# Kernel tuning notes

Measured on AMD Instinct MI355X. Metric: run time of the kernel, lower is better.

Reference implementation:

```python
import jax, jax.numpy as jnp
import numpy as np

N, E = 100000, 1200000
IN, HC = 3, 64
FC1, FC2, FC3, OUT = 64, 32, 16, 3
BN_EPS = 1e-5


def _lin(key, fan_in, fan_out):
    # kaiming-uniform-ish init, zero bias (as in parameter_init)
    bound = np.sqrt(6.0 / fan_in)
    w = jax.random.uniform(key, (fan_in, fan_out), minval=-bound, maxval=bound, dtype=jnp.float32)
    return w, jnp.zeros((fan_out,), jnp.float32)


def setup_inputs() -> dict:
    key = jax.random.key(0)
    ks = jax.random.split(key, 16)
    x = jax.random.normal(ks[0], (N, IN), dtype=jnp.float32)
    edge_index = jax.random.randint(ks[1], (2, E), 0, N, dtype=jnp.int64)
    d = {"x": x, "edge_index": edge_index}
    # EdgeConv MLPs: Linear(2*c_in, hc) -> ReLU -> Linear(hc, hc)
    d["w1a"], d["b1a"] = _lin(ks[2], 2 * IN, HC)
    d["w1b"], d["b1b"] = _lin(ks[3], HC, HC)
    d["w2a"], d["b2a"] = _lin(ks[4], 2 * HC, HC)
    d["w2b"], d["b2b"] = _lin(ks[5], HC, HC)
    d["w3a"], d["b3a"] = _lin(ks[6], 2 * HC, HC)
    d["w3b"], d["b3b"] = _lin(ks[7], HC, HC)
    # BatchNorm (eval mode) params per layer: gamma, beta, running_mean, running_var
    for i in (1, 2, 3):
        d[f"bn{i}_g"] = jnp.ones((HC,), jnp.float32)
        d[f"bn{i}_b"] = jnp.zeros((HC,), jnp.float32)
        d[f"bn{i}_m"] = jnp.zeros((HC,), jnp.float32)
        d[f"bn{i}_v"] = jnp.ones((HC,), jnp.float32)
    # dense head
    d["lw1"], d["lb1"] = _lin(ks[8], HC, FC1)
    d["lw2"], d["lb2"] = _lin(ks[9], FC1, FC2)
    d["lw3"], d["lb3"] = _lin(ks[10], FC2, FC3)
    d["lw4"], d["lb4"] = _lin(ks[11], FC3, OUT)
    return d


def _edge_conv(x, src, dst, wa, ba, wb, bb):
    # PyG EdgeConv: message = mlp(cat[x_i, x_j - x_i]), max-aggregated at target i
    x_i = x[dst]                              # [E, C]
    x_j = x[src]                              # [E, C]
    h = jnp.concatenate([x_i, x_j - x_i], axis=-1)   # [E, 2C]
    h = jax.nn.relu(h @ wa + ba) @ wb + bb           # [E, HC]
    agg = jax.ops.segment_max(h, dst, num_segments=x.shape[0])
    return jnp.where(jnp.isfinite(agg), agg, 0.0)    # isolated nodes -> 0


def _bn(x, g, b, m, v):
    return (x - m) * jax.lax.rsqrt(v + BN_EPS) * g + b


def reference(x, edge_index,
              w1a, b1a, w1b, b1b, w2a, b2a, w2b, b2b, w3a, b3a, w3b, b3b,
              bn1_g, bn1_b, bn1_m, bn1_v, bn2_g, bn2_b, bn2_m, bn2_v,
              bn3_g, bn3_b, bn3_m, bn3_v,
              lw1, lb1, lw2, lb2, lw3, lb3, lw4, lb4):
    src, dst = edge_index[0], edge_index[1]
    h = _edge_conv(x, src, dst, w1a, b1a, w1b, b1b)
    h = jax.nn.relu(_bn(h, bn1_g, bn1_b, bn1_m, bn1_v))
    h = _edge_conv(h, src, dst, w2a, b2a, w2b, b2b)
    h = jax.nn.relu(_bn(h, bn2_g, bn2_b, bn2_m, bn2_v))
    h = _edge_conv(h, src, dst, w3a, b3a, w3b, b3b)
    h = jax.nn.relu(_bn(h, bn3_g, bn3_b, bn3_m, bn3_v))
    h = jax.nn.relu(h @ lw1 + lb1)
    h = jax.nn.relu(h @ lw2 + lb2)
    h = jax.nn.relu(h @ lw3 + lb3)
    return h @ lw4 + lb4
```

## Files before the change

kernel.cpp:

```cpp
#include <hip/hip_runtime.h>

#define CAP 64
#define BN_EPS 1e-5f

typedef _Float16 f16;
typedef _Float16 half8 __attribute__((ext_vector_type(8)));
typedef float f32x4 __attribute__((ext_vector_type(4)));

__global__ __launch_bounds__(256) void build_buckets(
    const int* __restrict__ ei, int E,
    int* __restrict__ deg, int* __restrict__ bucket)
{
    int e = blockIdx.x * blockDim.x + threadIdx.x;
    if (e >= E) return;
    int src = ei[e];
    int dst = ei[E + e];
    int slot = atomicAdd(&deg[dst], 1);
    if (slot < CAP) bucket[dst * CAP + slot] = src;
}

__global__ __launch_bounds__(256) void uv_kernel(
    const float* __restrict__ feat, int ldf, int K, int N,
    const float* __restrict__ wa, const float* __restrict__ ba,
    f16* __restrict__ U, f16* __restrict__ V)
{
    __shared__ float Wlds[2][64][64];
    __shared__ float blds[64];
    int tid = threadIdx.x;
    for (int idx = tid; idx < 2 * K * 64; idx += blockDim.x) {
        int half = idx / (K * 64);
        int rem = idx - half * (K * 64);
        int k = rem >> 6, o = rem & 63;
        float wB = wa[(K + k) * 64 + o];
        Wlds[half][k][o] = (half == 0) ? (wa[k * 64 + o] - wB) : wB;
    }
    if (tid < 64) blds[tid] = ba[tid];
    __syncthreads();

    int t = blockIdx.x * blockDim.x + tid;
    if (t >= 2 * N) return;
    int node = t >> 1, half = t & 1;

    float acc[64];
    #pragma unroll
    for (int o = 0; o < 64; ++o) acc[o] = (half == 0) ? blds[o] : 0.f;

    const float* f = feat + (long)node * ldf;
    for (int k = 0; k < K; ++k) {
        float c = f[k];
        #pragma unroll
        for (int o = 0; o < 64; ++o) acc[o] = fmaf(c, Wlds[half][k][o], acc[o]);
    }
    f16* dstp = (half == 0 ? U : V) + (long)node * 64;
    #pragma unroll
    for (int o = 0; o < 64; o += 8) {
        half8 h;
        #pragma unroll
        for (int j = 0; j < 8; ++j) h[j] = (f16)acc[o + j];
        *(half8*)(dstp + o) = h;
    }
}

__global__ __launch_bounds__(256) void node_kernel(
    const f16* __restrict__ U, const f16* __restrict__ V,
    const int* __restrict__ deg, const int* __restrict__ bucket,
    const float* __restrict__ wb, const float* __restrict__ bb,
    const float* __restrict__ bng, const float* __restrict__ bnb,
    const float* __restrict__ bnm, const float* __restrict__ bnv,
    int N, float* __restrict__ Fout)
{
    const int lane = threadIdx.x & 63;
    const int r16 = lane >> 4, c16 = lane & 15;
    const int wid = (blockIdx.x * blockDim.x + threadIdx.x) >> 6;
    const int nwaves = (gridDim.x * blockDim.x) >> 6;

    half8 bfrag[8];
    #pragma unroll
    for (int ct = 0; ct < 4; ++ct)
        #pragma unroll
        for (int s = 0; s < 2; ++s) {
            half8 h;
            #pragma unroll
            for (int j = 0; j < 8; ++j) {
                int k = 32 * s + 8 * r16 + j;
                h[j] = (f16)wb[k * 64 + 16 * ct + c16];
            }
            bfrag[ct * 2 + s] = h;
        }

    const float bbv = bb[lane];
    const float g = bng[lane], be = bnb[lane];
    const float rs = rsqrtf(bnv[lane] + BN_EPS), mm = bnm[lane];

    int chunk = (N + nwaves - 1) / nwaves;
    int n0 = wid * chunk;
    int n1 = n0 + chunk; if (n1 > N) n1 = N;
    if (n0 >= n1) return;

    int dval = 0;
    if (lane < n1 - n0) dval = deg[n0 + lane];
    dval = dval > CAP ? CAP : dval;

    int bkt_cur = bucket[(long)n0 * CAP + c16];
    int np = (n0 + 1 < n1) ? n0 + 1 : n0;
    int bkt_nxt = bucket[(long)np * CAP + c16];

    unsigned s0u = (unsigned)bkt_cur < (unsigned)N ? (unsigned)bkt_cur : 0u;
    const half8* vr = (const half8*)(V + (long)s0u * 64);
    half8 vA = vr[r16], vB = vr[4 + r16];
    const half8* ur = (const half8*)(U + (long)n0 * 64);
    half8 uA = ur[r16], uB = ur[4 + r16];

    for (int node = n0; node < n1; ++node) {
        unsigned s1u = (unsigned)bkt_nxt < (unsigned)N ? (unsigned)bkt_nxt : 0u;
        const half8* vr1 = (const half8*)(V + (long)s1u * 64);
        half8 vA2 = vr1[r16], vB2 = vr1[4 + r16];
        int nn = (node + 2 < n1) ? node + 2 : n1 - 1;
        int bkt_fut = bucket[(long)nn * CAP + c16];
        int np1 = (node + 1 < n1) ? node + 1 : node;
        const half8* ur1 = (const half8*)(U + (long)np1 * 64);
        half8 uA2 = ur1[r16], uB2 = ur1[4 + r16];

        int d = __shfl(dval, node - n0);

        float m0 = -INFINITY, m1 = -INFINITY, m2 = -INFINITY, m3 = -INFINITY;
        int ntile = (d + 15) >> 4;

        if (ntile > 0) {
            half8 a0 = vA + uA;
            half8 a1 = vB + uB;
            #pragma unroll
            for (int j = 0; j < 8; ++j) {
                a0[j] = a0[j] > (f16)0 ? a0[j] : (f16)0;
                a1[j] = a1[j] > (f16)0 ? a1[j] : (f16)0;
            }
            const f32x4 z = {0.f, 0.f, 0.f, 0.f};
            #pragma unroll
            for (int ct = 0; ct < 4; ++ct) {
                f32x4 acc = __builtin_amdgcn_mfma_f32_16x16x32_f16(a0, bfrag[ct * 2 + 0], z, 0, 0, 0);
                acc = __builtin_amdgcn_mfma_f32_16x16x32_f16(a1, bfrag[ct * 2 + 1], acc, 0, 0, 0);
                float mx = -INFINITY;
                #pragma unroll
                for (int r = 0; r < 4; ++r) {
                    int row = r16 * 4 + r;
                    float val = (row < d) ? acc[r] : -INFINITY;
                    mx = fmaxf(mx, val);
                }
                mx = fmaxf(mx, __shfl_xor(mx, 16));
                mx = fmaxf(mx, __shfl_xor(mx, 32));
                if (ct == 0) m0 = fmaxf(m0, mx);
                else if (ct == 1) m1 = fmaxf(m1, mx);
                else if (ct == 2) m2 = fmaxf(m2, mx);
                else m3 = fmaxf(m3, mx);
            }
        }
        for (int t = 1; t < ntile; ++t) {
            int bkt = bucket[(long)node * CAP + t * 16 + c16];
            unsigned su = (unsigned)bkt < (unsigned)N ? (unsigned)bkt : 0u;
            const half8* vrt = (const half8*)(V + (long)su * 64);
            half8 a0 = vrt[r16] + uA;
            half8 a1 = vrt[4 + r16] + uB;
            #pragma unroll
            for (int j = 0; j < 8; ++j) {
                a0[j] = a0[j] > (f16)0 ? a0[j] : (f16)0;
                a1[j] = a1[j] > (f16)0 ? a1[j] : (f16)0;
            }
            const f32x4 z = {0.f, 0.f, 0.f, 0.f};
            #pragma unroll
            for (int ct = 0; ct < 4; ++ct) {
                f32x4 acc = __builtin_amdgcn_mfma_f32_16x16x32_f16(a0, bfrag[ct * 2 + 0], z, 0, 0, 0);
                acc = __builtin_amdgcn_mfma_f32_16x16x32_f16(a1, bfrag[ct * 2 + 1], acc, 0, 0, 0);
                float mx = -INFINITY;
                #pragma unroll
                for (int r = 0; r < 4; ++r) {
                    int row = t * 16 + r16 * 4 + r;
                    float val = (row < d) ? acc[r] : -INFINITY;
                    mx = fmaxf(mx, val);
                }
                mx = fmaxf(mx, __shfl_xor(mx, 16));
                mx = fmaxf(mx, __shfl_xor(mx, 32));
                if (ct == 0) m0 = fmaxf(m0, mx);
                else if (ct == 1) m1 = fmaxf(m1, mx);
                else if (ct == 2) m2 = fmaxf(m2, mx);
                else m3 = fmaxf(m3, mx);
            }
        }

        float sel = (r16 == 0) ? m0 : (r16 == 1) ? m1 : (r16 == 2) ? m2 : m3;
        float aggv = (d > 0) ? sel + bbv : 0.f;
        float bn = (aggv - mm) * rs * g + be;
        Fout[(long)node * 64 + lane] = fmaxf(bn, 0.f);

        vA = vA2; vB = vB2; uA = uA2; uB = uB2; bkt_nxt = bkt_fut;
    }
}

__global__ __launch_bounds__(256) void head_kernel(
    const float* __restrict__ F,
    const float* __restrict__ lw1, const float* __restrict__ lb1,
    const float* __restrict__ lw2, const float* __restrict__ lb2,
    const float* __restrict__ lw3, const float* __restrict__ lb3,
    const float* __restrict__ lw4, const float* __restrict__ lb4,
    int N, float* __restrict__ out)
{
    __shared__ float W1[64][64];
    __shared__ float W2[64][32];
    __shared__ float W3[32][16];
    __shared__ float W4[16][3];
    __shared__ float B1[64], B2[32], B3[16], B4[3];
    int tid = threadIdx.x;
    for (int i = tid; i < 64 * 64; i += blockDim.x) W1[i >> 6][i & 63] = lw1[i];
    for (int i = tid; i < 64 * 32; i += blockDim.x) W2[i >> 5][i & 31] = lw2[i];
    for (int i = tid; i < 32 * 16; i += blockDim.x) W3[i >> 4][i & 15] = lw3[i];
    for (int i = tid; i < 16 * 3;  i += blockDim.x) W4[i / 3][i % 3]  = lw4[i];
    if (tid < 64) B1[tid] = lb1[tid];
    if (tid < 32) B2[tid] = lb2[tid];
    if (tid < 16) B3[tid] = lb3[tid];
    if (tid < 3)  B4[tid] = lb4[tid];
    __syncthreads();

    int n = blockIdx.x * blockDim.x + tid;
    if (n >= N) return;
    const float* f = F + (long)n * 64;

    float h1[64];
    #pragma unroll
    for (int o = 0; o < 64; ++o) h1[o] = B1[o];
    for (int k = 0; k < 64; ++k) {
        float c = f[k];
        #pragma unroll
        for (int o = 0; o < 64; ++o) h1[o] = fmaf(c, W1[k][o], h1[o]);
    }
    float h2[32];
    #pragma unroll
    for (int o = 0; o < 32; ++o) h2[o] = B2[o];
    #pragma unroll
    for (int k = 0; k < 64; ++k) {
        float c = fmaxf(h1[k], 0.f);
        #pragma unroll
        for (int o = 0; o < 32; ++o) h2[o] = fmaf(c, W2[k][o], h2[o]);
    }
    float h3[16];
    #pragma unroll
    for (int o = 0; o < 16; ++o) h3[o] = B3[o];
    #pragma unroll
    for (int k = 0; k < 32; ++k) {
        float c = fmaxf(h2[k], 0.f);
        #pragma unroll
        for (int o = 0; o < 16; ++o) h3[o] = fmaf(c, W3[k][o], h3[o]);
    }
    float o0 = B4[0], o1 = B4[1], o2 = B4[2];
    #pragma unroll
    for (int k = 0; k < 16; ++k) {
        float c = fmaxf(h3[k], 0.f);
        o0 = fmaf(c, W4[k][0], o0);
        o1 = fmaf(c, W4[k][1], o1);
        o2 = fmaf(c, W4[k][2], o2);
    }
    out[(long)n * 3 + 0] = o0;
    out[(long)n * 3 + 1] = o1;
    out[(long)n * 3 + 2] = o2;
}

extern "C" void kernel_launch(void* const* d_in, const int* in_sizes, int n_in,
                              void* d_out, int out_size, void* d_ws, size_t ws_size,
                              hipStream_t stream)
{
    const float* x   = (const float*)d_in[0];
    const int*   ei  = (const int*)d_in[1];
    int N = in_sizes[0] / 3;
    int E = in_sizes[1] / 2;

    const float* w1a = (const float*)d_in[2];  const float* b1a = (const float*)d_in[3];
    const float* w1b = (const float*)d_in[4];  const float* b1b = (const float*)d_in[5];
    const float* w2a = (const float*)d_in[6];  const float* b2a = (const float*)d_in[7];
    const float* w2b = (const float*)d_in[8];  const float* b2b = (const float*)d_in[9];
    const float* w3a = (const float*)d_in[10]; const float* b3a = (const float*)d_in[11];
    const float* w3b = (const float*)d_in[12]; const float* b3b = (const float*)d_in[13];
    const float* bn1g = (const float*)d_in[14]; const float* bn1b = (const float*)d_in[15];
    const float* bn1m = (const float*)d_in[16]; const float* bn1v = (const float*)d_in[17];
    const float* bn2g = (const float*)d_in[18]; const float* bn2b = (const float*)d_in[19];
    const float* bn2m = (const float*)d_in[20]; const float* bn2v = (const float*)d_in[21];
    const float* bn3g = (const float*)d_in[22]; const float* bn3b = (const float*)d_in[23];
    const float* bn3m = (const float*)d_in[24]; const float* bn3v = (const float*)d_in[25];
    const float* lw1 = (const float*)d_in[26]; const float* lb1 = (const float*)d_in[27];
    const float* lw2 = (const float*)d_in[28]; const float* lb2 = (const float*)d_in[29];
    const float* lw3 = (const float*)d_in[30]; const float* lb3 = (const float*)d_in[31];
    const float* lw4 = (const float*)d_in[32]; const float* lb4 = (const float*)d_in[33];
    float* out = (float*)d_out;

    char* ws = (char*)d_ws;
    size_t off = 0;
    auto alloc = [&](size_t bytes) { void* p = ws + off; off += (bytes + 255) & ~(size_t)255; return p; };
    int*   deg    = (int*)  alloc((size_t)N * sizeof(int));
    int*   bucket = (int*)  alloc((size_t)N * CAP * sizeof(int));
    f16*   U      = (f16*)  alloc((size_t)N * 64 * sizeof(f16));
    f16*   V      = (f16*)  alloc((size_t)N * 64 * sizeof(f16));
    float* F      = (float*)alloc((size_t)N * 64 * sizeof(float));
    (void)ws_size; (void)n_in; (void)out_size;

    hipMemsetAsync(deg, 0, (size_t)N * sizeof(int), stream);
    build_buckets<<<(E + 255) / 256, 256, 0, stream>>>(ei, E, deg, bucket);

    int uv_grid   = (2 * N + 255) / 256;
    int node_blocks = 2048;
    int nd_grid   = (N + 255) / 256;

    uv_kernel<<<uv_grid, 256, 0, stream>>>(x, 3, 3, N, w1a, b1a, U, V);
    node_kernel<<<node_blocks, 256, 0, stream>>>(U, V, deg, bucket, w1b, b1b,
                                                 bn1g, bn1b, bn1m, bn1v, N, F);
    uv_kernel<<<uv_grid, 256, 0, stream>>>(F, 64, 64, N, w2a, b2a, U, V);
    node_kernel<<<node_blocks, 256, 0, stream>>>(U, V, deg, bucket, w2b, b2b,
                                                 bn2g, bn2b, bn2m, bn2v, N, F);
    uv_kernel<<<uv_grid, 256, 0, stream>>>(F, 64, 64, N, w3a, b3a, U, V);
    node_kernel<<<node_blocks, 256, 0, stream>>>(U, V, deg, bucket, w3b, b3b,
                                                 bn3g, bn3b, bn3m, bn3v, N, F);
    head_kernel<<<nd_grid, 256, 0, stream>>>(F, lw1, lb1, lw2, lb2, lw3, lb3,
                                             lw4, lb4, N, out);
}
```

Before: 551.2 us.

## Deepen gather prefetch to two nodes and move B fragments to LDS

The node kernel now prefetches V rows two nodes ahead and bucket indices three ahead, up from one and two, to hide gather latency. The wb B-fragments move from registers into a shared-memory array read per MFMA, and launch bounds request 8 blocks per CU. Together these aim to free VGPRs for higher occupancy despite the extra prefetch registers. The cost is LDS reads on every MFMA, a block-level sync, and a possible spill risk under the tighter register budget.

Result: slower. 1.002 ms (+81.8%).

```diff
diff --git a/kernel.cpp b/kernel.cpp
--- a/kernel.cpp
+++ b/kernel.cpp
@@ -61,7 +61,7 @@
     }
 }
 
-__global__ __launch_bounds__(256) void node_kernel(
+__global__ __launch_bounds__(256, 8) void node_kernel(
     const f16* __restrict__ U, const f16* __restrict__ V,
     const int* __restrict__ deg, const int* __restrict__ bucket,
     const float* __restrict__ wb, const float* __restrict__ bb,
@@ -74,19 +74,20 @@
     const int wid = (blockIdx.x * blockDim.x + threadIdx.x) >> 6;
     const int nwaves = (gridDim.x * blockDim.x) >> 6;
 
-    half8 bfrag[8];
-    #pragma unroll
-    for (int ct = 0; ct < 4; ++ct)
-        #pragma unroll
-        for (int s = 0; s < 2; ++s) {
-            half8 h;
-            #pragma unroll
-            for (int j = 0; j < 8; ++j) {
-                int k = 32 * s + 8 * r16 + j;
-                h[j] = (f16)wb[k * 64 + 16 * ct + c16];
-            }
-            bfrag[ct * 2 + s] = h;
+    __shared__ half8 WB[8][64];
+    for (int idx = threadIdx.x; idx < 8 * 64; idx += blockDim.x) {
+        int f = idx >> 6, l = idx & 63;
+        int lr = l >> 4, lc = l & 15;
+        int s = f & 1, ct = f >> 1;
+        half8 h;
+        #pragma unroll
+        for (int j = 0; j < 8; ++j) {
+            int k = 32 * s + 8 * lr + j;
+            h[j] = (f16)wb[k * 64 + 16 * ct + lc];
         }
+        WB[f][l] = h;
+    }
+    __syncthreads();
 
     const float bbv = bb[lane];
     const float g = bng[lane], be = bnb[lane];
@@ -101,25 +102,28 @@
     if (lane < n1 - n0) dval = deg[n0 + lane];
     dval = dval > CAP ? CAP : dval;
 
-    int bkt_cur = bucket[(long)n0 * CAP + c16];
-    int np = (n0 + 1 < n1) ? n0 + 1 : n0;
-    int bkt_nxt = bucket[(long)np * CAP + c16];
-
-    unsigned s0u = (unsigned)bkt_cur < (unsigned)N ? (unsigned)bkt_cur : 0u;
-    const half8* vr = (const half8*)(V + (long)s0u * 64);
-    half8 vA = vr[r16], vB = vr[4 + r16];
-    const half8* ur = (const half8*)(U + (long)n0 * 64);
-    half8 uA = ur[r16], uB = ur[4 + r16];
+    auto nclamp = [&](int n) { return n < n1 ? n : n1 - 1; };
+
+    int bkt0 = bucket[(long)n0 * CAP + c16];
+    int bkt1 = bucket[(long)nclamp(n0 + 1) * CAP + c16];
+    int bkt2 = bucket[(long)nclamp(n0 + 2) * CAP + c16];
+
+    unsigned s0 = (unsigned)bkt0 < (unsigned)N ? (unsigned)bkt0 : 0u;
+    unsigned s1 = (unsigned)bkt1 < (unsigned)N ? (unsigned)bkt1 : 0u;
+    const half8* vp0 = (const half8*)(V + (long)s0 * 64);
+    const half8* vp1 = (const half8*)(V + (long)s1 * 64);
+    half8 v0A = vp0[r16], v0B = vp0[4 + r16];
+    half8 v1A = vp1[r16], v1B = vp1[4 + r16];
+    const half8* up0 = (const half8*)(U + (long)n0 * 64);
+    half8 u0A = up0[r16], u0B = up0[4 + r16];
 
     for (int node = n0; node < n1; ++node) {
-        unsigned s1u = (unsigned)bkt_nxt < (unsigned)N ? (unsigned)bkt_nxt : 0u;
-        const half8* vr1 = (const half8*)(V + (long)s1u * 64);
-        half8 vA2 = vr1[r16], vB2 = vr1[4 + r16];
-        int nn = (node + 2 < n1) ? node + 2 : n1 - 1;
-        int bkt_fut = bucket[(long)nn * CAP + c16];
-        int np1 = (node + 1 < n1) ? node + 1 : node;
-        const half8* ur1 = (const half8*)(U + (long)np1 * 64);
-        half8 uA2 = ur1[r16], uB2 = ur1[4 + r16];
+        unsigned s2 = (unsigned)bkt2 < (unsigned)N ? (unsigned)bkt2 : 0u;
+        const half8* vp2 = (const half8*)(V + (long)s2 * 64);
+        half8 v2A = vp2[r16], v2B = vp2[4 + r16];
+        int bkt3 = bucket[(long)nclamp(node + 3) * CAP + c16];
+        const half8* up1 = (const half8*)(U + (long)nclamp(node + 1) * 64);
+        half8 u1A = up1[r16], u1B = up1[4 + r16];
 
         int d = __shfl(dval, node - n0);
 
@@ -127,8 +131,8 @@
         int ntile = (d + 15) >> 4;
 
         if (ntile > 0) {
-            half8 a0 = vA + uA;
-            half8 a1 = vB + uB;
+            half8 a0 = v0A + u0A;
+            half8 a1 = v0B + u0B;
             #pragma unroll
             for (int j = 0; j < 8; ++j) {
                 a0[j] = a0[j] > (f16)0 ? a0[j] : (f16)0;
@@ -137,8 +141,8 @@
             const f32x4 z = {0.f, 0.f, 0.f, 0.f};
             #pragma unroll
             for (int ct = 0; ct < 4; ++ct) {
-                f32x4 acc = __builtin_amdgcn_mfma_f32_16x16x32_f16(a0, bfrag[ct * 2 + 0], z, 0, 0, 0);
-                acc = __builtin_amdgcn_mfma_f32_16x16x32_f16(a1, bfrag[ct * 2 + 1], acc, 0, 0, 0);
+                f32x4 acc = __builtin_amdgcn_mfma_f32_16x16x32_f16(a0, WB[ct * 2 + 0][lane], z, 0, 0, 0);
+                acc = __builtin_amdgcn_mfma_f32_16x16x32_f16(a1, WB[ct * 2 + 1][lane], acc, 0, 0, 0);
                 float mx = -INFINITY;
                 #pragma unroll
                 for (int r = 0; r < 4; ++r) {
@@ -158,8 +162,8 @@
             int bkt = bucket[(long)node * CAP + t * 16 + c16];
             unsigned su = (unsigned)bkt < (unsigned)N ? (unsigned)bkt : 0u;
             const half8* vrt = (const half8*)(V + (long)su * 64);
-            half8 a0 = vrt[r16] + uA;
-            half8 a1 = vrt[4 + r16] + uB;
+            half8 a0 = vrt[r16] + u0A;
+            half8 a1 = vrt[4 + r16] + u0B;
             #pragma unroll
             for (int j = 0; j < 8; ++j) {
                 a0[j] = a0[j] > (f16)0 ? a0[j] : (f16)0;
@@ -168,8 +172,8 @@
             const f32x4 z = {0.f, 0.f, 0.f, 0.f};
             #pragma unroll
             for (int ct = 0; ct < 4; ++ct) {
-                f32x4 acc = __builtin_amdgcn_mfma_f32_16x16x32_f16(a0, bfrag[ct * 2 + 0], z, 0, 0, 0);
-                acc = __builtin_amdgcn_mfma_f32_16x16x32_f16(a1, bfrag[ct * 2 + 1], acc, 0, 0, 0);
+                f32x4 acc = __builtin_amdgcn_mfma_f32_16x16x32_f16(a0, WB[ct * 2 + 0][lane], z, 0, 0, 0);
+                acc = __builtin_amdgcn_mfma_f32_16x16x32_f16(a1, WB[ct * 2 + 1][lane], acc, 0, 0, 0);
                 float mx = -INFINITY;
                 #pragma unroll
                 for (int r = 0; r < 4; ++r) {
@@ -191,7 +195,9 @@
         float bn = (aggv - mm) * rs * g + be;
         Fout[(long)node * 64 + lane] = fmaxf(bn, 0.f);
 
-        vA = vA2; vB = vB2; uA = uA2; uB = uB2; bkt_nxt = bkt_fut;
+        v0A = v1A; v0B = v1B; v1A = v2A; v1B = v2B;
+        u0A = u1A; u0B = u1B;
+        bkt2 = bkt3;
     }
 }
 
```
